# Kernel optimization log

Hardware: AMD Instinct MI355X
Metric: run time of the kernel (lower is better)

The kernel has to match this reference:

```python
import jax, jax.numpy as jnp
import numpy as np

M, K, N, E, TOPK = 256, 1024, 2048, 64, 8  # tokens, hidden, expert out dim, experts, top-k


def setup_inputs() -> dict:
    key = jax.random.key(0)
    k1, k2, k3, k4, k5 = jax.random.split(key, 5)
    A = jax.random.normal(k1, (M, K), jnp.float32)
    B = jax.random.normal(k2, (E, N, K), jnp.float32) * 0.02  # expert weights [E,N,K]
    B_bias = jax.random.normal(k3, (E, N), jnp.float32)
    topk_weights = jax.random.uniform(k4, (M, TOPK), jnp.float32)
    # Balanced routing: each expert gets exactly M*TOPK/E assignments so the
    # static-shape sorted grouped-GEMM below is exact (mirrors moe_align_block_size).
    flat = jax.random.permutation(k5, jnp.arange(M * TOPK, dtype=jnp.int32) % E)
    topk_ids = flat.reshape(M, TOPK)
    return {"A": A, "B": B, "B_bias": B_bias, "topk_weights": topk_weights, "topk_ids": topk_ids}


def reference(A, B, B_bias, topk_weights, topk_ids):
    # C[m, t, :] = (A[m] @ B[e].T + bias[e]) * topk_weights[m, t],  e = topk_ids[m, t]
    M_, K_ = A.shape
    E_, N_, _ = B.shape
    topk = topk_ids.shape[1]
    L = M_ * topk
    cap = L // E_  # exact per-expert count (balanced routing)
    flat_e = topk_ids.reshape(-1)                      # [L]
    order = jnp.argsort(flat_e)                        # stable sort by expert id
    tok = order // topk                                # source token row per sorted slot
    A_sorted = A[tok].reshape(E_, cap, K_)             # token gather, grouped by expert
    y = jnp.einsum('eck,enk->ecn', A_sorted, B)        # grouped GEMM
    y = y + B_bias[:, None, :]                         # bias add
    w = topk_weights.reshape(-1)[order]                # routing weight per sorted slot
    y = y.reshape(L, N_) * w[:, None]                  # routed-weight multiply
    out = jnp.zeros((L, N_), A.dtype).at[order].set(y) # scatter back to token order
    return out.reshape(M_, topk, N_)
```

## Files before the change

### kernel.cpp

```cpp
#include <hip/hip_runtime.h>
#include <hip/hip_bf16.h>

#define M_TOK 256
#define K_DIM 1024
#define N_DIM 2048
#define NE    64
#define TOPKK 8
#define L_ROWS (M_TOK * TOPKK)
#define CAP    (L_ROWS / NE)

#define BN  128
#define BK  64
#define LDK (BK + 8)

typedef __bf16 bf16x8 __attribute__((ext_vector_type(8)));
typedef float  f32x4  __attribute__((ext_vector_type(4)));

__global__ void route_kernel(const int* __restrict__ ids, int* __restrict__ slots) {
    int e    = blockIdx.x;
    int lane = threadIdx.x;
    int base = 0;
    for (int c = 0; c < L_ROWS; c += 64) {
        int slot = c + lane;
        bool match = (ids[slot] == e);
        unsigned long long mask = __ballot(match);
        int pos = __popcll(mask & ((1ULL << lane) - 1ULL));
        if (match) slots[e * CAP + base + pos] = slot;
        base += __popcll(mask);
    }
}

__device__ inline void cvt_store4(__bf16* dst, float4 v) {
    dst[0] = (__bf16)v.x; dst[1] = (__bf16)v.y;
    dst[2] = (__bf16)v.z; dst[3] = (__bf16)v.w;
}

__global__ __launch_bounds__(256, 2) void moe_gemm(
    const float* __restrict__ A,
    const float* __restrict__ B,
    const float* __restrict__ bias,
    const float* __restrict__ tw,
    const int*   __restrict__ slots,
    float*       __restrict__ out)
{
    const int e  = blockIdx.x >> 4;
    const int n0 = (blockIdx.x & 15) * BN;

    __shared__ __bf16 sA[32 * LDK];
    __shared__ __bf16 sB[BN * LDK];
    __shared__ int    sSlot[CAP];
    __shared__ float  sW[CAP];

    const int t = threadIdx.x;
    if (t < CAP) {
        int s = slots[e * CAP + t];
        sSlot[t] = s;
        sW[t]    = tw[s];
    }
    __syncthreads();

    const int rA = t >> 4;
    const int k4 = t & 15;

    const int tok0 = sSlot[rA] >> 3;
    const int tok1 = sSlot[rA + 16] >> 3;
    const float* aPtr0 = A + (size_t)tok0 * K_DIM + k4 * 4;
    const float* aPtr1 = A + (size_t)tok1 * K_DIM + k4 * 4;
    const float* bPtr  = B + ((size_t)e * N_DIM + n0 + rA) * K_DIM + k4 * 4;

    const int wv   = t >> 6;
    const int lane = t & 63;
    const int fr   = lane & 15;
    const int kg   = lane >> 4;

    f32x4 acc[2][2] = {{{0.f,0.f,0.f,0.f},{0.f,0.f,0.f,0.f}},
                       {{0.f,0.f,0.f,0.f},{0.f,0.f,0.f,0.f}}};

    for (int k0 = 0; k0 < K_DIM; k0 += BK) {
        float4 av0 = *(const float4*)(aPtr0 + k0);
        float4 av1 = *(const float4*)(aPtr1 + k0);
        float4 bv[8];
        #pragma unroll
        for (int i = 0; i < 8; i++)
            bv[i] = *(const float4*)(bPtr + (size_t)i * 16 * K_DIM + k0);

        cvt_store4(&sA[rA        * LDK + k4 * 4], av0);
        cvt_store4(&sA[(rA + 16) * LDK + k4 * 4], av1);
        #pragma unroll
        for (int i = 0; i < 8; i++)
            cvt_store4(&sB[(rA + i * 16) * LDK + k4 * 4], bv[i]);
        __syncthreads();

        #pragma unroll
        for (int kk = 0; kk < 2; kk++) {
            const int koff = kg * 8 + kk * 32;
            bf16x8 a0 = *(const bf16x8*)&sA[fr        * LDK + koff];
            bf16x8 a1 = *(const bf16x8*)&sA[(fr + 16) * LDK + koff];
            bf16x8 b0 = *(const bf16x8*)&sB[(wv * 32 + fr)      * LDK + koff];
            bf16x8 b1 = *(const bf16x8*)&sB[(wv * 32 + 16 + fr) * LDK + koff];
            acc[0][0] = __builtin_amdgcn_mfma_f32_16x16x32_bf16(a0, b0, acc[0][0], 0, 0, 0);
            acc[0][1] = __builtin_amdgcn_mfma_f32_16x16x32_bf16(a0, b1, acc[0][1], 0, 0, 0);
            acc[1][0] = __builtin_amdgcn_mfma_f32_16x16x32_bf16(a1, b0, acc[1][0], 0, 0, 0);
            acc[1][1] = __builtin_amdgcn_mfma_f32_16x16x32_bf16(a1, b1, acc[1][1], 0, 0, 0);
        }
        __syncthreads();
    }

    const int nl0 = n0 + wv * 32 + fr;
    const float bias0 = bias[(size_t)e * N_DIM + nl0];
    const float bias1 = bias[(size_t)e * N_DIM + nl0 + 16];

    #pragma unroll
    for (int mt = 0; mt < 2; mt++) {
        #pragma unroll
        for (int r = 0; r < 4; r++) {
            const int m    = mt * 16 + kg * 4 + r;
            const int slot = sSlot[m];
            const float wg = sW[m];
            out[(size_t)slot * N_DIM + nl0]      = (acc[mt][0][r] + bias0) * wg;
            out[(size_t)slot * N_DIM + nl0 + 16] = (acc[mt][1][r] + bias1) * wg;
        }
    }
}

extern "C" void kernel_launch(void* const* d_in, const int* in_sizes, int n_in,
                              void* d_out, int out_size, void* d_ws, size_t ws_size,
                              hipStream_t stream) {
    const float* A    = (const float*)d_in[0];
    const float* B    = (const float*)d_in[1];
    const float* bias = (const float*)d_in[2];
    const float* tw   = (const float*)d_in[3];
    const int*   ids  = (const int*)d_in[4];
    float* out  = (float*)d_out;
    int* slots  = (int*)d_ws;

    route_kernel<<<NE, 64, 0, stream>>>(ids, slots);
    moe_gemm<<<NE * 16, 256, 0, stream>>>(A, B, bias, tw, slots, out);
}
```

Measured before the change: 734.5 us.

## Load MFMA fragments directly from global memory with register double-buffering

Removes the shared-memory staging of A and B tiles and the two barriers per K step. Each lane now loads its own MFMA operand fragments straight from global memory, converts them to bf16 in registers, and prefetches the next 32-wide K chunk while computing the current one. Occupancy hint is raised to 4 blocks per SM. The cost is that A rows are read once per wave instead of once per block (4x redundant A traffic), and global loads use 32-byte-per-lane strided row accesses, which coalesce less well than the previous layout.

Result: slower. 755.0 us (+2.8%).

```diff
diff --git a/kernel.cpp b/kernel.cpp
--- a/kernel.cpp
+++ b/kernel.cpp
@@ -8,10 +8,7 @@
 #define TOPKK 8
 #define L_ROWS (M_TOK * TOPKK)
 #define CAP    (L_ROWS / NE)
-
-#define BN  128
-#define BK  64
-#define LDK (BK + 8)
+#define BN    128
 
 typedef __bf16 bf16x8 __attribute__((ext_vector_type(8)));
 typedef float  f32x4  __attribute__((ext_vector_type(4)));
@@ -30,12 +27,35 @@
     }
 }
 
-__device__ inline void cvt_store4(__bf16* dst, float4 v) {
-    dst[0] = (__bf16)v.x; dst[1] = (__bf16)v.y;
-    dst[2] = (__bf16)v.z; dst[3] = (__bf16)v.w;
+__device__ inline bf16x8 cvt8(float4 lo, float4 hi) {
+    bf16x8 r;
+    r[0] = (__bf16)lo.x; r[1] = (__bf16)lo.y; r[2] = (__bf16)lo.z; r[3] = (__bf16)lo.w;
+    r[4] = (__bf16)hi.x; r[5] = (__bf16)hi.y; r[6] = (__bf16)hi.z; r[7] = (__bf16)hi.w;
+    return r;
 }
 
-__global__ __launch_bounds__(256, 2) void moe_gemm(
+struct Chunk { float4 v[8]; };
+
+__device__ inline void load_chunk(Chunk& c, const float* a0, const float* a1,
+                                  const float* b0, const float* b1, int k) {
+    c.v[0] = *(const float4*)(a0 + k);     c.v[1] = *(const float4*)(a0 + k + 4);
+    c.v[2] = *(const float4*)(a1 + k);     c.v[3] = *(const float4*)(a1 + k + 4);
+    c.v[4] = *(const float4*)(b0 + k);     c.v[5] = *(const float4*)(b0 + k + 4);
+    c.v[6] = *(const float4*)(b1 + k);     c.v[7] = *(const float4*)(b1 + k + 4);
+}
+
+__device__ inline void mfma_step(const Chunk& c, f32x4 acc[2][2]) {
+    bf16x8 fa0 = cvt8(c.v[0], c.v[1]);
+    bf16x8 fa1 = cvt8(c.v[2], c.v[3]);
+    bf16x8 fb0 = cvt8(c.v[4], c.v[5]);
+    bf16x8 fb1 = cvt8(c.v[6], c.v[7]);
+    acc[0][0] = __builtin_amdgcn_mfma_f32_16x16x32_bf16(fa0, fb0, acc[0][0], 0, 0, 0);
+    acc[0][1] = __builtin_amdgcn_mfma_f32_16x16x32_bf16(fa0, fb1, acc[0][1], 0, 0, 0);
+    acc[1][0] = __builtin_amdgcn_mfma_f32_16x16x32_bf16(fa1, fb0, acc[1][0], 0, 0, 0);
+    acc[1][1] = __builtin_amdgcn_mfma_f32_16x16x32_bf16(fa1, fb1, acc[1][1], 0, 0, 0);
+}
+
+__global__ __launch_bounds__(256, 4) void moe_gemm(
     const float* __restrict__ A,
     const float* __restrict__ B,
     const float* __restrict__ bias,
@@ -46,65 +66,35 @@
     const int e  = blockIdx.x >> 4;
     const int n0 = (blockIdx.x & 15) * BN;
 
-    __shared__ __bf16 sA[32 * LDK];
-    __shared__ __bf16 sB[BN * LDK];
-    __shared__ int    sSlot[CAP];
-    __shared__ float  sW[CAP];
-
-    const int t = threadIdx.x;
-    if (t < CAP) {
-        int s = slots[e * CAP + t];
-        sSlot[t] = s;
-        sW[t]    = tw[s];
-    }
-    __syncthreads();
-
-    const int rA = t >> 4;
-    const int k4 = t & 15;
-
-    const int tok0 = sSlot[rA] >> 3;
-    const int tok1 = sSlot[rA + 16] >> 3;
-    const float* aPtr0 = A + (size_t)tok0 * K_DIM + k4 * 4;
-    const float* aPtr1 = A + (size_t)tok1 * K_DIM + k4 * 4;
-    const float* bPtr  = B + ((size_t)e * N_DIM + n0 + rA) * K_DIM + k4 * 4;
-
+    const int t    = threadIdx.x;
     const int wv   = t >> 6;
     const int lane = t & 63;
     const int fr   = lane & 15;
     const int kg   = lane >> 4;
 
+    const int slot0 = slots[e * CAP + fr];
+    const int slot1 = slots[e * CAP + fr + 16];
+    const float* a0p = A + (size_t)(slot0 >> 3) * K_DIM + kg * 8;
+    const float* a1p = A + (size_t)(slot1 >> 3) * K_DIM + kg * 8;
+
+    const int nr = n0 + wv * 32 + fr;
+    const float* b0p = B + ((size_t)e * N_DIM + nr) * K_DIM + kg * 8;
+    const float* b1p = b0p + (size_t)16 * K_DIM;
+
     f32x4 acc[2][2] = {{{0.f,0.f,0.f,0.f},{0.f,0.f,0.f,0.f}},
                        {{0.f,0.f,0.f,0.f},{0.f,0.f,0.f,0.f}}};
 
-    for (int k0 = 0; k0 < K_DIM; k0 += BK) {
-        float4 av0 = *(const float4*)(aPtr0 + k0);
-        float4 av1 = *(const float4*)(aPtr1 + k0);
-        float4 bv[8];
+    Chunk cur, nxt;
+    load_chunk(cur, a0p, a1p, b0p, b1p, 0);
+
+    #pragma unroll 2
+    for (int k = 32; k < K_DIM; k += 32) {
+        load_chunk(nxt, a0p, a1p, b0p, b1p, k);
+        mfma_step(cur, acc);
         #pragma unroll
-        for (int i = 0; i < 8; i++)
-            bv[i] = *(const float4*)(bPtr + (size_t)i * 16 * K_DIM + k0);
-
-        cvt_store4(&sA[rA        * LDK + k4 * 4], av0);
-        cvt_store4(&sA[(rA + 16) * LDK + k4 * 4], av1);
-        #pragma unroll
-        for (int i = 0; i < 8; i++)
-            cvt_store4(&sB[(rA + i * 16) * LDK + k4 * 4], bv[i]);
-        __syncthreads();
-
-        #pragma unroll
-        for (int kk = 0; kk < 2; kk++) {
-            const int koff = kg * 8 + kk * 32;
-            bf16x8 a0 = *(const bf16x8*)&sA[fr        * LDK + koff];
-            bf16x8 a1 = *(const bf16x8*)&sA[(fr + 16) * LDK + koff];
-            bf16x8 b0 = *(const bf16x8*)&sB[(wv * 32 + fr)      * LDK + koff];
-            bf16x8 b1 = *(const bf16x8*)&sB[(wv * 32 + 16 + fr) * LDK + koff];
-            acc[0][0] = __builtin_amdgcn_mfma_f32_16x16x32_bf16(a0, b0, acc[0][0], 0, 0, 0);
-            acc[0][1] = __builtin_amdgcn_mfma_f32_16x16x32_bf16(a0, b1, acc[0][1], 0, 0, 0);
-            acc[1][0] = __builtin_amdgcn_mfma_f32_16x16x32_bf16(a1, b0, acc[1][0], 0, 0, 0);
-            acc[1][1] = __builtin_amdgcn_mfma_f32_16x16x32_bf16(a1, b1, acc[1][1], 0, 0, 0);
-        }
-        __syncthreads();
+        for (int i = 0; i < 8; i++) cur.v[i] = nxt.v[i];
     }
+    mfma_step(cur, acc);
 
     const int nl0 = n0 + wv * 32 + fr;
     const float bias0 = bias[(size_t)e * N_DIM + nl0];
@@ -115,8 +105,8 @@
         #pragma unroll
         for (int r = 0; r < 4; r++) {
             const int m    = mt * 16 + kg * 4 + r;
-            const int slot = sSlot[m];
-            const float wg = sW[m];
+            const int slot = slots[e * CAP + m];
+            const float wg = tw[slot];
             out[(size_t)slot * N_DIM + nl0]      = (acc[mt][0][r] + bias0) * wg;
             out[(size_t)slot * N_DIM + nl0 + 16] = (acc[mt][1][r] + bias1) * wg;
         }
```
